# Optimization experiments

Measured on AMD Instinct MI355X. Metric: run time of the kernel, lower is better.

Reference implementation:

```python
import jax, jax.numpy as jnp
import numpy as np

N_NODES = 50000
N_EDGES = 1600000
F_IN = 128
NUM_CLASSES = 40


def _gat_conv(x, src, dst, W, a_src, a_dst, b, concat):
    # x: [N, Fin], W: [Fin, H*C], a_src/a_dst: [H, C], b: [H*C] or [C]
    H, C = a_src.shape
    N = x.shape[0]
    h = (x @ W).reshape(N, H, C)                       # [N,H,C]
    al_s = jnp.einsum('nhc,hc->nh', h, a_src)          # [N,H]
    al_d = jnp.einsum('nhc,hc->nh', h, a_dst)          # [N,H]
    e = jax.nn.leaky_relu(al_s[src] + al_d[dst], 0.2)  # [E,H]
    # segment softmax over destination nodes
    m = jax.ops.segment_max(e, dst, num_segments=N)    # [N,H]
    ex = jnp.exp(e - m[dst])
    s = jax.ops.segment_sum(ex, dst, num_segments=N)   # [N,H]
    alpha = ex / s[dst]                                # [E,H]
    out = jax.ops.segment_sum(h[src] * alpha[:, :, None], dst, num_segments=N)  # [N,H,C]
    if concat:
        return out.reshape(N, H * C) + b
    return out.mean(axis=1) + b


def setup_inputs() -> dict:
    key = jax.random.key(0)
    ks = jax.random.split(key, 12)
    s = 0.1
    inp = {
        'x': jax.random.normal(ks[0], (N_NODES, F_IN), jnp.float32),
        'edge_index': jax.random.randint(ks[1], (2, N_EDGES), 0, N_NODES, jnp.int64),
        # conv1: 128 -> 16, heads=4, concat
        'W1': jax.random.normal(ks[2], (F_IN, 4 * 16), jnp.float32) * s,
        'a1s': jax.random.normal(ks[3], (4, 16), jnp.float32) * s,
        'a1d': jax.random.normal(ks[4], (4, 16), jnp.float32) * s,
        'b1': jnp.zeros((4 * 16,), jnp.float32),
        # conv2: 64 -> 16, heads=4, concat
        'W2': jax.random.normal(ks[5], (64, 4 * 16), jnp.float32) * s,
        'a2s': jax.random.normal(ks[6], (4, 16), jnp.float32) * s,
        'a2d': jax.random.normal(ks[7], (4, 16), jnp.float32) * s,
        'b2': jnp.zeros((4 * 16,), jnp.float32),
        # conv3: 64 -> num_classes, heads=6, mean
        'W3': jax.random.normal(ks[8], (64, 6 * NUM_CLASSES), jnp.float32) * s,
        'a3s': jax.random.normal(ks[9], (6, NUM_CLASSES), jnp.float32) * s,
        'a3d': jax.random.normal(ks[10], (6, NUM_CLASSES), jnp.float32) * s,
        'b3': jnp.zeros((NUM_CLASSES,), jnp.float32),
    }
    return inp


def reference(x, edge_index, W1, a1s, a1d, b1, W2, a2s, a2d, b2, W3, a3s, a3d, b3):
    N = x.shape[0]
    loop = jnp.arange(N, dtype=edge_index.dtype)
    src = jnp.concatenate([edge_index[0], loop])  # add_self_loops=True (PyG default)
    dst = jnp.concatenate([edge_index[1], loop])
    h = jax.nn.elu(_gat_conv(x, src, dst, W1, a1s, a1d, b1, concat=True))
    h = jax.nn.elu(_gat_conv(h, src, dst, W2, a2s, a2d, b2, concat=True))
    h = jax.nn.elu(_gat_conv(h, src, dst, W3, a3s, a3d, b3, concat=False))
    return jax.nn.log_softmax(h, axis=1)
```

## Files before the change

### kernel.cpp

```cpp
#include <hip/hip_runtime.h>
#include <math.h>

#define N_NODES 50000
#define N_EDGES 1600000
#define NB      391
#define CHUNK   8192
#define NCHUNK  196
#define LOG2E   1.44269504088896340736f

typedef __attribute__((ext_vector_type(2))) float v2f;
typedef __attribute__((ext_vector_type(4))) float f32x4;
typedef __attribute__((ext_vector_type(8))) __bf16 bf16x8;

__device__ __forceinline__ float lrelu02(float x) { return fmaxf(x, 0.2f * x); }
__device__ __forceinline__ float elu1(float x)    { return x > 0.f ? x : __expf(x) - 1.f; }
__device__ __forceinline__ float exp2_fast(float x) {
    float r; asm("v_exp_f32 %0, %1" : "=v"(r) : "v"(x)); return r;
}

__device__ __forceinline__ unsigned short f2bf(float f) {
    unsigned int u = __float_as_uint(f);
    return (unsigned short)((u + 0x7fffu + ((u >> 16) & 1u)) >> 16);
}
__device__ __forceinline__ float bf2f(unsigned short s) {
    return __uint_as_float((unsigned int)s << 16);
}
__device__ __forceinline__ float2 bfp2(unsigned int u) {
    float2 r;
    r.x = __uint_as_float(u << 16);
    r.y = __uint_as_float(u & 0xffff0000u);
    return r;
}

union BF8U { unsigned short u[8]; bf16x8 v; };
__device__ __forceinline__ bf16x8 cvt8(float4 a, float4 b) {
    BF8U r;
    r.u[0] = f2bf(a.x); r.u[1] = f2bf(a.y); r.u[2] = f2bf(a.z); r.u[3] = f2bf(a.w);
    r.u[4] = f2bf(b.x); r.u[5] = f2bf(b.y); r.u[6] = f2bf(b.z); r.u[7] = f2bf(b.w);
    return r.v;
}

__global__ __launch_bounds__(256) void bucket2_gemm_kernel(
        const int* __restrict__ ei, int* __restrict__ bcur, unsigned int* __restrict__ stage,
        const float* __restrict__ x, const float* __restrict__ W,
        const float* __restrict__ a_s, const float* __restrict__ a_d,
        unsigned short* __restrict__ h, float* __restrict__ al_s, float* __restrict__ al_d) {
    __shared__ alignas(16) char smem[37472];
    const int tid = threadIdx.x;
    if (blockIdx.x < NCHUNK) {
        unsigned int* vals = (unsigned int*)smem;
        int* hist  = (int*)(smem + 32768);
        int* cnt2  = hist + NB;
        int* gbase = cnt2 + NB;
        for (int i = tid; i < NB; i += 256) { hist[i] = 0; cnt2[i] = 0; }
        __syncthreads();
        const int e0 = blockIdx.x * CHUNK;
        int n = N_EDGES - e0; if (n > CHUNK) n = CHUNK;
        const int4* s4 = (const int4*)ei + (e0 >> 2);
        const int4* d4 = (const int4*)(ei + N_EDGES) + (e0 >> 2);
        for (int i = tid; i < (n >> 2); i += 256) {
            int4 s = s4[i], d = d4[i];
            vals[4 * i + 0] = ((unsigned int)d.x << 16) | (unsigned int)s.x;
            vals[4 * i + 1] = ((unsigned int)d.y << 16) | (unsigned int)s.y;
            vals[4 * i + 2] = ((unsigned int)d.z << 16) | (unsigned int)s.z;
            vals[4 * i + 3] = ((unsigned int)d.w << 16) | (unsigned int)s.w;
            atomicAdd(&hist[d.x >> 7], 1);
            atomicAdd(&hist[d.y >> 7], 1);
            atomicAdd(&hist[d.z >> 7], 1);
            atomicAdd(&hist[d.w >> 7], 1);
        }
        __syncthreads();
        for (int b = tid; b < NB; b += 256)
            if (hist[b]) gbase[b] = atomicAdd(&bcur[b * 16], hist[b]);
        __syncthreads();
        for (int i = tid; i < n; i += 256) {
            unsigned int v = vals[i];
            int b = v >> 23;
            int r = atomicAdd(&cnt2[b], 1);
            stage[gbase[b] + r] = v & 0x7FFFFFu;
        }
    } else {
        constexpr int FIN = 128, KS = FIN / 32;
        unsigned short* Wl = (unsigned short*)smem;
        unsigned short (*ot)[64] = (unsigned short(*)[64])(smem + 16384);
        const int bid = blockIdx.x - NCHUNK;
        for (int i = tid; i < FIN * 64; i += 256) {
            int ks = i >> 11;
            int rem = i & 2047;
            int c = rem >> 5, r = rem & 31;
            Wl[i] = f2bf(W[(ks * 32 + r) * 64 + c]);
        }
        __syncthreads();

        const int wv = tid >> 6, l = tid & 63;
        const int m = l & 15, g = l >> 4;
        const int n0 = bid * 64;
        int row = n0 + wv * 16 + m;
        if (row > N_NODES - 1) row = N_NODES - 1;
        const float* xr = x + (size_t)row * FIN + g * 8;

        f32x4 acc[4] = {};
#pragma unroll
        for (int ks = 0; ks < KS; ++ks) {
            float4 xa = *(const float4*)(xr + ks * 32);
            float4 xb = *(const float4*)(xr + ks * 32 + 4);
            bf16x8 af = cvt8(xa, xb);
            const unsigned short* wp = &Wl[ks * 2048 + g * 8];
#pragma unroll
            for (int t = 0; t < 4; ++t) {
                bf16x8 bf = *(const bf16x8*)(wp + (t * 16 + m) * 32);
                acc[t] = __builtin_amdgcn_mfma_f32_16x16x32_bf16(af, bf, acc[t], 0, 0, 0);
            }
        }
#pragma unroll
        for (int t = 0; t < 4; ++t)
#pragma unroll
            for (int j = 0; j < 4; ++j)
                ot[wv * 16 + g * 4 + j][t * 16 + m] = f2bf(acc[t][j]);
        __syncthreads();

        int vrows = N_NODES - n0; if (vrows > 64) vrows = 64;
        {
            unsigned int* ph = (unsigned int*)(h + (size_t)n0 * 64);
            for (int i = tid; i < vrows * 32; i += 256) {
                int r = i >> 5, c = i & 31;
                ph[i] = *(const unsigned int*)&ot[r][c * 2];
            }
        }
        {
            int node = tid >> 2, hd = tid & 3;
            if (node < vrows) {
                const float* as = a_s + hd * 16;
                const float* ad = a_d + hd * 16;
                float s1 = 0.f, s2 = 0.f;
#pragma unroll
                for (int c = 0; c < 16; c += 2) {
                    unsigned int q = *(const unsigned int*)&ot[node][hd * 16 + c];
                    float2 p = bfp2(q);
                    s1 = fmaf(p.x, as[c], s1);     s2 = fmaf(p.x, ad[c], s2);
                    s1 = fmaf(p.y, as[c + 1], s1); s2 = fmaf(p.y, ad[c + 1], s2);
                }
                al_s[(n0 + node) * 4 + hd] = s1 * LOG2E;
                al_d[(n0 + node) * 4 + hd] = s2 * LOG2E;
            }
        }
    }
}

__global__ __launch_bounds__(256) void gemm_albf64_kernel(const unsigned short* __restrict__ xb,
                               const float* __restrict__ W,
                               const float* __restrict__ a_s, const float* __restrict__ a_d,
                               unsigned short* __restrict__ h,
                               float* __restrict__ al_s, float* __restrict__ al_d) {
    __shared__ alignas(16) unsigned short Wl[2 * 64 * 32];
    __shared__ alignas(16) unsigned short ot[64][64];
    const int tid = threadIdx.x;
    for (int i = tid; i < 64 * 64; i += 256) {
        int ks = i >> 11;
        int rem = i & 2047;
        int c = rem >> 5, r = rem & 31;
        Wl[i] = f2bf(W[(ks * 32 + r) * 64 + c]);
    }
    __syncthreads();

    const int wv = tid >> 6, l = tid & 63;
    const int m = l & 15, g = l >> 4;
    const int n0 = blockIdx.x * 64;
    int row = n0 + wv * 16 + m;
    if (row > N_NODES - 1) row = N_NODES - 1;
    const unsigned short* xr = xb + (size_t)row * 64 + g * 8;

    f32x4 acc[4] = {};
#pragma unroll
    for (int ks = 0; ks < 2; ++ks) {
        bf16x8 af = *(const bf16x8*)(xr + ks * 32);
        const unsigned short* wp = &Wl[ks * 2048 + g * 8];
#pragma unroll
        for (int t = 0; t < 4; ++t) {
            bf16x8 bf = *(const bf16x8*)(wp + (t * 16 + m) * 32);
            acc[t] = __builtin_amdgcn_mfma_f32_16x16x32_bf16(af, bf, acc[t], 0, 0, 0);
        }
    }
#pragma unroll
    for (int t = 0; t < 4; ++t)
#pragma unroll
        for (int j = 0; j < 4; ++j)
            ot[wv * 16 + g * 4 + j][t * 16 + m] = f2bf(acc[t][j]);
    __syncthreads();

    int vrows = N_NODES - n0; if (vrows > 64) vrows = 64;
    {
        unsigned int* ph = (unsigned int*)(h + (size_t)n0 * 64);
        for (int i = tid; i < vrows * 32; i += 256) {
            int r = i >> 5, c = i & 31;
            ph[i] = *(const unsigned int*)&ot[r][c * 2];
        }
    }
    {
        int node = tid >> 2, hd = tid & 3;
        if (node < vrows) {
            const float* as = a_s + hd * 16;
            const float* ad = a_d + hd * 16;
            float s1 = 0.f, s2 = 0.f;
#pragma unroll
            for (int c = 0; c < 16; c += 2) {
                unsigned int q = *(const unsigned int*)&ot[node][hd * 16 + c];
                float2 p = bfp2(q);
                s1 = fmaf(p.x, as[c], s1);     s2 = fmaf(p.x, ad[c], s2);
                s1 = fmaf(p.y, as[c + 1], s1); s2 = fmaf(p.y, ad[c + 1], s2);
            }
            al_s[(n0 + node) * 4 + hd] = s1 * LOG2E;
            al_d[(n0 + node) * 4 + hd] = s2 * LOG2E;
        }
    }
}

__global__ __launch_bounds__(256) void gemm80_kernel(const unsigned short* __restrict__ xb,
                              const float* __restrict__ W,
                              const float* __restrict__ a_s, const float* __restrict__ a_d,
                              unsigned int* __restrict__ h8,
                              float* __restrict__ al_s, float* __restrict__ al_d) {
    __shared__ alignas(16) unsigned short Wl[2 * 80 * 32];
    __shared__ alignas(16) unsigned short ot[64][80];
    const int tid = threadIdx.x;
    const int nb = blockIdx.x / 3, third = blockIdx.x % 3;
    const int cb = third * 80;
    for (int i = tid; i < 2 * 80 * 32; i += 256) {
        int ks = i / 2560;
        int rem = i - ks * 2560;
        int c = rem >> 5, r = rem & 31;
        Wl[i] = f2bf(W[(ks * 32 + r) * 240 + cb + c]);
    }
    __syncthreads();

    const int wv = tid >> 6, l = tid & 63;
    const int m = l & 15, g = l >> 4;
    const int n0 = nb * 64;
    int row = n0 + wv * 16 + m;
    if (row > N_NODES - 1) row = N_NODES - 1;
    const unsigned short* xr = xb + (size_t)row * 64 + g * 8;

    f32x4 acc[5] = {};
#pragma unroll
    for (int ks = 0; ks < 2; ++ks) {
        bf16x8 af = *(const bf16x8*)(xr + ks * 32);
        const unsigned short* wp = &Wl[ks * 2560 + g * 8];
#pragma unroll
        for (int t = 0; t < 5; ++t) {
            bf16x8 bf = *(const bf16x8*)(wp + (t * 16 + m) * 32);
            acc[t] = __builtin_amdgcn_mfma_f32_16x16x32_bf16(af, bf, acc[t], 0, 0, 0);
        }
    }
#pragma unroll
    for (int t = 0; t < 5; ++t)
#pragma unroll
        for (int j = 0; j < 4; ++j)
            ot[wv * 16 + g * 4 + j][t * 16 + m] = f2bf(acc[t][j]);
    __syncthreads();

    int vrows = N_NODES - n0; if (vrows > 64) vrows = 64;
    {
        for (int i = tid; i < vrows * 20; i += 256) {
            int r = i / 20, c = i - r * 20;
            uint2 q = *(const uint2*)&ot[r][c * 4];
            float2 p0 = bfp2(q.x), p1 = bfp2(q.y);
            int lo = __builtin_amdgcn_cvt_pk_fp8_f32(p0.x, p0.y, 0, false);
            unsigned int packed = (unsigned int)__builtin_amdgcn_cvt_pk_fp8_f32(p1.x, p1.y, lo, true);
            h8[(size_t)(n0 + r) * 64 + cb / 4 + c] = packed;
        }
        if (third == 0) {
            for (int i = tid; i < vrows * 4; i += 256)
                h8[(size_t)(n0 + (i >> 2)) * 64 + 60 + (i & 3)] = 0;
        }
    }
    for (int t = tid; t < vrows * 2; t += 256) {
        int node = t >> 1, hh = t & 1;
        int hd = third * 2 + hh;
        const unsigned short* rp = &ot[node][hh * 40];
        const float* as = a_s + hd * 40;
        const float* ad = a_d + hd * 40;
        float s1 = 0.f, s2 = 0.f;
#pragma unroll
        for (int c = 0; c < 40; c += 2) {
            unsigned int q = *(const unsigned int*)(rp + c);
            float2 p = bfp2(q);
            s1 = fmaf(p.x, as[c], s1);     s2 = fmaf(p.x, ad[c], s2);
            s1 = fmaf(p.y, as[c + 1], s1); s2 = fmaf(p.y, ad[c + 1], s2);
        }
        al_s[(n0 + node) * 6 + hd] = s1 * LOG2E;
        al_d[(n0 + node) * 6 + hd] = s2 * LOG2E;
    }
}

__global__ __launch_bounds__(256) void bcnt_kernel(const int* __restrict__ ei, int* __restrict__ bcnt) {
    __shared__ int hist[NB];
    const int t = threadIdx.x;
    for (int i = t; i < NB; i += 256) hist[i] = 0;
    __syncthreads();
    const int e0 = blockIdx.x * CHUNK;
    int n = N_EDGES - e0; if (n > CHUNK) n = CHUNK;
    const int4* d4 = (const int4*)(ei + N_EDGES) + (e0 >> 2);
    for (int i = t; i < (n >> 2); i += 256) {
        int4 d = d4[i];
        atomicAdd(&hist[d.x >> 7], 1);
        atomicAdd(&hist[d.y >> 7], 1);
        atomicAdd(&hist[d.z >> 7], 1);
        atomicAdd(&hist[d.w >> 7], 1);
    }
    __syncthreads();
    for (int b = t; b < NB; b += 256)
        if (hist[b]) atomicAdd(&bcnt[b], hist[b]);
}

__global__ void scan391_kernel(const int* __restrict__ bcnt, int* __restrict__ bbase,
                               int* __restrict__ bcur) {
    __shared__ int wtot[8];
    int b = threadIdx.x;
    int lane = b & 63, w = b >> 6;
    int v = (b < NB) ? bcnt[b] : 0;
    int sc = v;
#pragma unroll
    for (int off = 1; off < 64; off <<= 1) {
        int u = __shfl_up(sc, off);
        if (lane >= off) sc += u;
    }
    if (lane == 63) wtot[w] = sc;
    __syncthreads();
    int add = 0;
    for (int k = 0; k < w; ++k) add += wtot[k];
    int excl = sc - v + add;
    if (b < NB) { bbase[b] = excl; bcur[b * 16] = excl; }
    if (b == 0) bbase[NB] = N_EDGES;
}

__global__ __launch_bounds__(256) void place2_kernel(const unsigned int* __restrict__ stage,
                                                     const int* __restrict__ bbase,
                                                     int* __restrict__ rowptr,
                                                     unsigned short* __restrict__ csr) {
    __shared__ int hist[128];
    __shared__ int cur[128];
    __shared__ int wt[2];
    const int b = blockIdx.x;
    const int n0 = b * 128;
    const int t = threadIdx.x;
    const int base = bbase[b];
    const int endp = bbase[b + 1];
    if (t < 128) hist[t] = 0;
    __syncthreads();
    for (int i = base + t; i < endp; i += 256)
        atomicAdd(&hist[stage[i] >> 16], 1);
    __syncthreads();
    int v = 0, sc = 0;
    if (t < 128) {
        v = hist[t];
        int lane = t & 63, w = t >> 6;
        sc = v;
#pragma unroll
        for (int off = 1; off < 64; off <<= 1) {
            int u = __shfl_up(sc, off);
            if (lane >= off) sc += u;
        }
        if (lane == 63) wt[w] = sc;
    }
    __syncthreads();
    if (t < 128) {
        int add = (t >= 64) ? wt[0] : 0;
        int excl = sc - v + add;
        int n = n0 + t;
        if (n <= N_NODES) rowptr[n] = base + excl;
        cur[t] = base + excl;
    }
    __syncthreads();
    for (int i = base + t; i < endp; i += 256) {
        unsigned int e = stage[i];
        int pos = atomicAdd(&cur[e >> 16], 1);
        csr[pos] = (unsigned short)(e & 0xFFFFu);
    }
}

__global__ void agg64_kernel(const int* __restrict__ rowptr, const unsigned short* __restrict__ csr_src,
                             const float* __restrict__ al_s, const float* __restrict__ al_d,
                             const unsigned short* __restrict__ hb, const float* __restrict__ b,
                             unsigned short* __restrict__ xn) {
    const int node = blockIdx.x * 4 + (threadIdx.x >> 6);
    const int lane = threadIdx.x & 63;
    const int eg = lane >> 3;
    const int cl = lane & 7;
    const int c0 = cl * 8;
    const int hd = cl >> 1;
    const float ald = al_d[(unsigned)(node * 4 + hd)];
    const int beg = rowptr[node], end = rowptr[node + 1];
    float denom = 0.f;
    float a0 = 0.f, a1 = 0.f, a2 = 0.f, a3 = 0.f, a4 = 0.f, a5 = 0.f, a6 = 0.f, a7 = 0.f;
    auto accQ = [&](uint4 q, float w) {
        float2 p;
        p = bfp2(q.x); a0 = fmaf(w, p.x, a0); a1 = fmaf(w, p.y, a1);
        p = bfp2(q.y); a2 = fmaf(w, p.x, a2); a3 = fmaf(w, p.y, a3);
        p = bfp2(q.z); a4 = fmaf(w, p.x, a4); a5 = fmaf(w, p.y, a5);
        p = bfp2(q.w); a6 = fmaf(w, p.x, a6); a7 = fmaf(w, p.y, a7);
    };
    if (eg == 0) {
        float w = exp2_fast(lrelu02(al_s[(unsigned)(node * 4 + hd)] + ald));
        uint4 q = *(const uint4*)(hb + (unsigned)(node * 64 + c0));
        denom = w;
        accQ(q, w);
    }
    int j = beg + eg;
    for (; j + 24 < end; j += 32) {
        int s0 = csr_src[j], s1 = csr_src[j + 8], s2 = csr_src[j + 16], s3 = csr_src[j + 24];
        uint4 q0 = *(const uint4*)(hb + (unsigned)(s0 * 64 + c0));
        uint4 q1 = *(const uint4*)(hb + (unsigned)(s1 * 64 + c0));
        uint4 q2 = *(const uint4*)(hb + (unsigned)(s2 * 64 + c0));
        uint4 q3 = *(const uint4*)(hb + (unsigned)(s3 * 64 + c0));
        float w0 = exp2_fast(lrelu02(al_s[(unsigned)(s0 * 4 + hd)] + ald));
        float w1 = exp2_fast(lrelu02(al_s[(unsigned)(s1 * 4 + hd)] + ald));
        float w2 = exp2_fast(lrelu02(al_s[(unsigned)(s2 * 4 + hd)] + ald));
        float w3 = exp2_fast(lrelu02(al_s[(unsigned)(s3 * 4 + hd)] + ald));
        denom += (w0 + w1) + (w2 + w3);
        accQ(q0, w0); accQ(q1, w1); accQ(q2, w2); accQ(q3, w3);
    }
    for (; j < end; j += 8) {
        int s0 = csr_src[j];
        uint4 q0 = *(const uint4*)(hb + (unsigned)(s0 * 64 + c0));
        float w0 = exp2_fast(lrelu02(al_s[(unsigned)(s0 * 4 + hd)] + ald));
        denom += w0;
        accQ(q0, w0);
    }
    denom += __shfl_xor(denom, 8); denom += __shfl_xor(denom, 16); denom += __shfl_xor(denom, 32);
    a0 += __shfl_xor(a0, 8); a0 += __shfl_xor(a0, 16); a0 += __shfl_xor(a0, 32);
    a1 += __shfl_xor(a1, 8); a1 += __shfl_xor(a1, 16); a1 += __shfl_xor(a1, 32);
    a2 += __shfl_xor(a2, 8); a2 += __shfl_xor(a2, 16); a2 += __shfl_xor(a2, 32);
    a3 += __shfl_xor(a3, 8); a3 += __shfl_xor(a3, 16); a3 += __shfl_xor(a3, 32);
    a4 += __shfl_xor(a4, 8); a4 += __shfl_xor(a4, 16); a4 += __shfl_xor(a4, 32);
    a5 += __shfl_xor(a5, 8); a5 += __shfl_xor(a5, 16); a5 += __shfl_xor(a5, 32);
    a6 += __shfl_xor(a6, 8); a6 += __shfl_xor(a6, 16); a6 += __shfl_xor(a6, 32);
    a7 += __shfl_xor(a7, 8); a7 += __shfl_xor(a7, 16); a7 += __shfl_xor(a7, 32);
    if (lane < 8) {
        float r = 1.f / denom;
        float4 bv0 = *(const float4*)(b + c0);
        float4 bv1 = *(const float4*)(b + c0 + 4);
        uint4 pk;
        pk.x = (unsigned int)f2bf(elu1(fmaf(a0, r, bv0.x)))
             | ((unsigned int)f2bf(elu1(fmaf(a1, r, bv0.y))) << 16);
        pk.y = (unsigned int)f2bf(elu1(fmaf(a2, r, bv0.z)))
             | ((unsigned int)f2bf(elu1(fmaf(a3, r, bv0.w))) << 16);
        pk.z = (unsigned int)f2bf(elu1(fmaf(a4, r, bv1.x)))
             | ((unsigned int)f2bf(elu1(fmaf(a5, r, bv1.y))) << 16);
        pk.w = (unsigned int)f2bf(elu1(fmaf(a6, r, bv1.z)))
             | ((unsigned int)f2bf(elu1(fmaf(a7, r, bv1.w))) << 16);
        *(uint4*)(xn + (unsigned)(node * 64 + c0)) = pk;
    }
}

__global__ void agg240_kernel(const int* __restrict__ rowptr, const unsigned short* __restrict__ csr_src,
                              const float* __restrict__ al_s, const float* __restrict__ al_d,
                              const unsigned int* __restrict__ h8, const float* __restrict__ b3,
                              float* __restrict__ y) {
    __shared__ float sh[4][240];
    const int wv_id = threadIdx.x >> 6;
    const int node = blockIdx.x * 4 + wv_id;
    const int lane = threadIdx.x & 63;
    const int eg = lane >> 5;
    const int cl = lane & 31;
    const int u0 = cl * 2;
    int hd = cl / 5; if (hd > 5) hd = 5;
    const float ald = al_d[(unsigned)(node * 6 + hd)];
    const int beg = rowptr[node], end = rowptr[node + 1];
    float denom = 0.f;
    float acc[8] = {0.f, 0.f, 0.f, 0.f, 0.f, 0.f, 0.f, 0.f};
    auto acc8 = [&](uint2 q, float w) {
        v2f p0 = __builtin_amdgcn_cvt_pk_f32_fp8((int)q.x, false);
        v2f p1 = __builtin_amdgcn_cvt_pk_f32_fp8((int)q.x, true);
        v2f p2 = __builtin_amdgcn_cvt_pk_f32_fp8((int)q.y, false);
        v2f p3 = __builtin_amdgcn_cvt_pk_f32_fp8((int)q.y, true);
        acc[0] = fmaf(w, p0.x, acc[0]); acc[1] = fmaf(w, p0.y, acc[1]);
        acc[2] = fmaf(w, p1.x, acc[2]); acc[3] = fmaf(w, p1.y, acc[3]);
        acc[4] = fmaf(w, p2.x, acc[4]); acc[5] = fmaf(w, p2.y, acc[5]);
        acc[6] = fmaf(w, p3.x, acc[6]); acc[7] = fmaf(w, p3.y, acc[7]);
    };
    if (eg == 0) {
        float w = exp2_fast(lrelu02(al_s[(unsigned)(node * 6 + hd)] + ald));
        uint2 q = *(const uint2*)(h8 + (unsigned)(node * 64) + u0);
        denom = w;
        acc8(q, w);
    }
    int j = beg + eg;
    for (; j + 6 < end; j += 8) {
        int s0 = csr_src[j], s1 = csr_src[j + 2], s2 = csr_src[j + 4], s3 = csr_src[j + 6];
        uint2 q0 = *(const uint2*)(h8 + (unsigned)(s0 * 64) + u0);
        uint2 q1 = *(const uint2*)(h8 + (unsigned)(s1 * 64) + u0);
        uint2 q2 = *(const uint2*)(h8 + (unsigned)(s2 * 64) + u0);
        uint2 q3 = *(const uint2*)(h8 + (unsigned)(s3 * 64) + u0);
        float w0 = exp2_fast(lrelu02(al_s[(unsigned)(s0 * 6 + hd)] + ald));
        float w1 = exp2_fast(lrelu02(al_s[(unsigned)(s1 * 6 + hd)] + ald));
        float w2 = exp2_fast(lrelu02(al_s[(unsigned)(s2 * 6 + hd)] + ald));
        float w3 = exp2_fast(lrelu02(al_s[(unsigned)(s3 * 6 + hd)] + ald));
        denom += (w0 + w1) + (w2 + w3);
        acc8(q0, w0); acc8(q1, w1); acc8(q2, w2); acc8(q3, w3);
    }
    for (; j < end; j += 2) {
        int s0 = csr_src[j];
        uint2 q0 = *(const uint2*)(h8 + (unsigned)(s0 * 64) + u0);
        float w0 = exp2_fast(lrelu02(al_s[(unsigned)(s0 * 6 + hd)] + ald));
        denom += w0;
        acc8(q0, w0);
    }
    denom += __shfl_xor(denom, 32);
#pragma unroll
    for (int i = 0; i < 8; ++i) acc[i] += __shfl_xor(acc[i], 32);
    if (eg == 0 && cl < 30) {
        float r = 1.f / denom;
        float* sp = &sh[wv_id][cl * 8];
#pragma unroll
        for (int i = 0; i < 8; ++i) sp[i] = acc[i] * r;
    }
    __syncthreads();
    float v;
    if (lane < 40) {
        const float* p = sh[wv_id];
        float s = 0.f;
#pragma unroll
        for (int hh = 0; hh < 6; ++hh) s += p[hh * 40 + lane];
        v = elu1(s * (1.f / 6.f) + b3[lane]);
    } else {
        v = -INFINITY;
    }
    float m = v;
#pragma unroll
    for (int o = 32; o > 0; o >>= 1) m = fmaxf(m, __shfl_xor(m, o));
    float ex = (lane < 40) ? __expf(v - m) : 0.f;
    float ssum = ex;
#pragma unroll
    for (int o = 32; o > 0; o >>= 1) ssum += __shfl_xor(ssum, o);
    if (lane < 40) y[(size_t)node * 40 + lane] = v - m - __logf(ssum);
}

extern "C" void kernel_launch(void* const* d_in, const int* in_sizes, int n_in,
                              void* d_out, int out_size, void* d_ws, size_t ws_size,
                              hipStream_t stream) {
    const float* x   = (const float*)d_in[0];
    const int*   ei  = (const int*)d_in[1];
    const float* W1  = (const float*)d_in[2];
    const float* a1s = (const float*)d_in[3];
    const float* a1d = (const float*)d_in[4];
    const float* b1  = (const float*)d_in[5];
    const float* W2  = (const float*)d_in[6];
    const float* a2s = (const float*)d_in[7];
    const float* a2d = (const float*)d_in[8];
    const float* b2  = (const float*)d_in[9];
    const float* W3  = (const float*)d_in[10];
    const float* a3s = (const float*)d_in[11];
    const float* a3d = (const float*)d_in[12];
    const float* b3  = (const float*)d_in[13];
    float* y = (float*)d_out;

    float* ws = (float*)d_ws;
    unsigned short* h_bf = (unsigned short*)ws;
    unsigned short* x_buf = (unsigned short*)(ws + 1600000);
    float* al_s    = ws + 4800000;
    float* al_d    = ws + 5100000;
    unsigned int* h8 = (unsigned int*)(ws + 5400000);
    int*   rowptr  = (int*)(ws + 8600000);
    unsigned short* csr_src = (unsigned short*)(ws + 8650008);
    unsigned int* stage = (unsigned int*)(ws + 9450008);
    int*   bcnt    = (int*)(ws + 11050008);
    int*   bbase   = (int*)(ws + 11050400);
    int*   bcur    = (int*)(ws + 11050792);

    const int agg_grid = N_NODES / 4;
    const int gemm_gx = (N_NODES + 63) / 64;

    hipMemsetAsync(bcnt, 0, NB * sizeof(int), stream);
    bcnt_kernel<<<NCHUNK, 256, 0, stream>>>(ei, bcnt);
    scan391_kernel<<<1, 512, 0, stream>>>(bcnt, bbase, bcur);
    bucket2_gemm_kernel<<<NCHUNK + gemm_gx, 256, 0, stream>>>(ei, bcur, stage,
                                                              x, W1, a1s, a1d, h_bf, al_s, al_d);
    place2_kernel<<<NB, 256, 0, stream>>>(stage, bbase, rowptr, csr_src);

    agg64_kernel<<<agg_grid, 256, 0, stream>>>(rowptr, csr_src, al_s, al_d, h_bf, b1, x_buf);

    gemm_albf64_kernel<<<gemm_gx, 256, 0, stream>>>(x_buf, W2, a2s, a2d, h_bf, al_s, al_d);
    agg64_kernel<<<agg_grid, 256, 0, stream>>>(rowptr, csr_src, al_s, al_d, h_bf, b2, x_buf);

    gemm80_kernel<<<gemm_gx * 3, 256, 0, stream>>>(x_buf, W3, a3s, a3d, h8, al_s, al_d);
    agg240_kernel<<<agg_grid, 256, 0, stream>>>(rowptr, csr_src, al_s, al_d, h8, b3, y);
}
```

Baseline: 335.4 us.

## Spread layer-1 GEMM blocks across bcnt, bucket, and place kernels

```diff
diff --git a/kernel.cpp b/kernel.cpp
--- a/kernel.cpp
+++ b/kernel.cpp
@@ -7,6 +7,9 @@
 #define CHUNK   8192
 #define NCHUNK  196
 #define LOG2E   1.44269504088896340736f
+#define G1A     150
+#define G1B     250
+#define G1C     382
 
 typedef __attribute__((ext_vector_type(2))) float v2f;
 typedef __attribute__((ext_vector_type(4))) float f32x4;
@@ -38,6 +41,126 @@
     r.u[0] = f2bf(a.x); r.u[1] = f2bf(a.y); r.u[2] = f2bf(a.z); r.u[3] = f2bf(a.w);
     r.u[4] = f2bf(b.x); r.u[5] = f2bf(b.y); r.u[6] = f2bf(b.z); r.u[7] = f2bf(b.w);
     return r.v;
+}
+
+__device__ __forceinline__ void gemm1_body(int bid, const float* __restrict__ x,
+        const float* __restrict__ W, const float* __restrict__ a_s, const float* __restrict__ a_d,
+        unsigned short* __restrict__ h, float* __restrict__ al_s, float* __restrict__ al_d,
+        char* smem) {
+    constexpr int FIN = 128, KS = FIN / 32;
+    unsigned short* Wl = (unsigned short*)smem;
+    unsigned short (*ot)[64] = (unsigned short(*)[64])(smem + 16384);
+    const int tid = threadIdx.x;
+    for (int i = tid; i < FIN * 64; i += 256) {
+        int ks = i >> 11;
+        int rem = i & 2047;
+        int c = rem >> 5, r = rem & 31;
+        Wl[i] = f2bf(W[(ks * 32 + r) * 64 + c]);
+    }
+    __syncthreads();
+
+    const int wv = tid >> 6, l = tid & 63;
+    const int m = l & 15, g = l >> 4;
+    const int n0 = bid * 64;
+    int row = n0 + wv * 16 + m;
+    if (row > N_NODES - 1) row = N_NODES - 1;
+    const float* xr = x + (size_t)row * FIN + g * 8;
+
+    f32x4 acc[4] = {};
+#pragma unroll
+    for (int ks = 0; ks < KS; ++ks) {
+        float4 xa = *(const float4*)(xr + ks * 32);
+        float4 xb = *(const float4*)(xr + ks * 32 + 4);
+        bf16x8 af = cvt8(xa, xb);
+        const unsigned short* wp = &Wl[ks * 2048 + g * 8];
+#pragma unroll
+        for (int t = 0; t < 4; ++t) {
+            bf16x8 bf = *(const bf16x8*)(wp + (t * 16 + m) * 32);
+            acc[t] = __builtin_amdgcn_mfma_f32_16x16x32_bf16(af, bf, acc[t], 0, 0, 0);
+        }
+    }
+#pragma unroll
+    for (int t = 0; t < 4; ++t)
+#pragma unroll
+        for (int j = 0; j < 4; ++j)
+            ot[wv * 16 + g * 4 + j][t * 16 + m] = f2bf(acc[t][j]);
+    __syncthreads();
+
+    int vrows = N_NODES - n0; if (vrows > 64) vrows = 64;
+    {
+        unsigned int* ph = (unsigned int*)(h + (size_t)n0 * 64);
+        for (int i = tid; i < vrows * 32; i += 256) {
+            int r = i >> 5, c = i & 31;
+            ph[i] = *(const unsigned int*)&ot[r][c * 2];
+        }
+    }
+    {
+        int node = tid >> 2, hd = tid & 3;
+        if (node < vrows) {
+            const float* as = a_s + hd * 16;
+            const float* ad = a_d + hd * 16;
+            float s1 = 0.f, s2 = 0.f;
+#pragma unroll
+            for (int c = 0; c < 16; c += 2) {
+                unsigned int q = *(const unsigned int*)&ot[node][hd * 16 + c];
+                float2 p = bfp2(q);
+                s1 = fmaf(p.x, as[c], s1);     s2 = fmaf(p.x, ad[c], s2);
+                s1 = fmaf(p.y, as[c + 1], s1); s2 = fmaf(p.y, ad[c + 1], s2);
+            }
+            al_s[(n0 + node) * 4 + hd] = s1 * LOG2E;
+            al_d[(n0 + node) * 4 + hd] = s2 * LOG2E;
+        }
+    }
+}
+
+__global__ __launch_bounds__(256) void bcnt_gemm_kernel(const int* __restrict__ ei,
+        int* __restrict__ bcnt,
+        const float* __restrict__ x, const float* __restrict__ W,
+        const float* __restrict__ a_s, const float* __restrict__ a_d,
+        unsigned short* __restrict__ h, float* __restrict__ al_s, float* __restrict__ al_d) {
+    __shared__ alignas(16) char smem[24576];
+    const int t = threadIdx.x;
+    if (blockIdx.x < NCHUNK) {
+        int* hist = (int*)smem;
+        for (int i = t; i < NB; i += 256) hist[i] = 0;
+        __syncthreads();
+        const int e0 = blockIdx.x * CHUNK;
+        int n = N_EDGES - e0; if (n > CHUNK) n = CHUNK;
+        const int4* d4 = (const int4*)(ei + N_EDGES) + (e0 >> 2);
+        for (int i = t; i < (n >> 2); i += 256) {
+            int4 d = d4[i];
+            atomicAdd(&hist[d.x >> 7], 1);
+            atomicAdd(&hist[d.y >> 7], 1);
+            atomicAdd(&hist[d.z >> 7], 1);
+            atomicAdd(&hist[d.w >> 7], 1);
+        }
+        __syncthreads();
+        for (int b = t; b < NB; b += 256)
+            if (hist[b]) atomicAdd(&bcnt[b], hist[b]);
+    } else {
+        gemm1_body(blockIdx.x - NCHUNK, x, W, a_s, a_d, h, al_s, al_d, smem);
+    }
+}
+
+__global__ void scan391_kernel(const int* __restrict__ bcnt, int* __restrict__ bbase,
+                               int* __restrict__ bcur) {
+    __shared__ int wtot[8];
+    int b = threadIdx.x;
+    int lane = b & 63, w = b >> 6;
+    int v = (b < NB) ? bcnt[b] : 0;
+    int sc = v;
+#pragma unroll
+    for (int off = 1; off < 64; off <<= 1) {
+        int u = __shfl_up(sc, off);
+        if (lane >= off) sc += u;
+    }
+    if (lane == 63) wtot[w] = sc;
+    __syncthreads();
+    int add = 0;
+    for (int k = 0; k < w; ++k) add += wtot[k];
+    int excl = sc - v + add;
+    if (b < NB) { bbase[b] = excl; bcur[b * 16] = excl; }
+    if (b == 0) bbase[NB] = N_EDGES;
 }
 
 __global__ __launch_bounds__(256) void bucket2_gemm_kernel(
@@ -80,70 +203,59 @@
             stage[gbase[b] + r] = v & 0x7FFFFFu;
         }
     } else {
-        constexpr int FIN = 128, KS = FIN / 32;
-        unsigned short* Wl = (unsigned short*)smem;
-        unsigned short (*ot)[64] = (unsigned short(*)[64])(smem + 16384);
-        const int bid = blockIdx.x - NCHUNK;
-        for (int i = tid; i < FIN * 64; i += 256) {
-            int ks = i >> 11;
-            int rem = i & 2047;
-            int c = rem >> 5, r = rem & 31;
-            Wl[i] = f2bf(W[(ks * 32 + r) * 64 + c]);
-        }
-        __syncthreads();
-
-        const int wv = tid >> 6, l = tid & 63;
-        const int m = l & 15, g = l >> 4;
-        const int n0 = bid * 64;
-        int row = n0 + wv * 16 + m;
-        if (row > N_NODES - 1) row = N_NODES - 1;
-        const float* xr = x + (size_t)row * FIN + g * 8;
-
-        f32x4 acc[4] = {};
-#pragma unroll
-        for (int ks = 0; ks < KS; ++ks) {
-            float4 xa = *(const float4*)(xr + ks * 32);
-            float4 xb = *(const float4*)(xr + ks * 32 + 4);
-            bf16x8 af = cvt8(xa, xb);
-            const unsigned short* wp = &Wl[ks * 2048 + g * 8];
-#pragma unroll
-            for (int t = 0; t < 4; ++t) {
-                bf16x8 bf = *(const bf16x8*)(wp + (t * 16 + m) * 32);
-                acc[t] = __builtin_amdgcn_mfma_f32_16x16x32_bf16(af, bf, acc[t], 0, 0, 0);
+        gemm1_body(blockIdx.x - NCHUNK + G1A, x, W, a_s, a_d, h, al_s, al_d, smem);
+    }
+}
+
+__global__ __launch_bounds__(256) void place2_gemm_kernel(
+        const unsigned int* __restrict__ stage, const int* __restrict__ bbase,
+        int* __restrict__ rowptr, unsigned short* __restrict__ csr,
+        const float* __restrict__ x, const float* __restrict__ W,
+        const float* __restrict__ a_s, const float* __restrict__ a_d,
+        unsigned short* __restrict__ h, float* __restrict__ al_s, float* __restrict__ al_d) {
+    __shared__ alignas(16) char smem[24576];
+    const int t = threadIdx.x;
+    if (blockIdx.x < NB) {
+        int* hist = (int*)smem;
+        int* cur  = hist + 128;
+        int* wt   = cur + 128;
+        const int b = blockIdx.x;
+        const int n0 = b * 128;
+        const int base = bbase[b];
+        const int endp = bbase[b + 1];
+        if (t < 128) hist[t] = 0;
+        __syncthreads();
+        for (int i = base + t; i < endp; i += 256)
+            atomicAdd(&hist[stage[i] >> 16], 1);
+        __syncthreads();
+        int v = 0, sc = 0;
+        if (t < 128) {
+            v = hist[t];
+            int lane = t & 63, w = t >> 6;
+            sc = v;
+#pragma unroll
+            for (int off = 1; off < 64; off <<= 1) {
+                int u = __shfl_up(sc, off);
+                if (lane >= off) sc += u;
             }
-        }
-#pragma unroll
-        for (int t = 0; t < 4; ++t)
-#pragma unroll
-            for (int j = 0; j < 4; ++j)
-                ot[wv * 16 + g * 4 + j][t * 16 + m] = f2bf(acc[t][j]);
-        __syncthreads();
-
-        int vrows = N_NODES - n0; if (vrows > 64) vrows = 64;
-        {
-            unsigned int* ph = (unsigned int*)(h + (size_t)n0 * 64);
-            for (int i = tid; i < vrows * 32; i += 256) {
-                int r = i >> 5, c = i & 31;
-                ph[i] = *(const unsigned int*)&ot[r][c * 2];
-            }
-        }
-        {
-            int node = tid >> 2, hd = tid & 3;
-            if (node < vrows) {
-                const float* as = a_s + hd * 16;
-                const float* ad = a_d + hd * 16;
-                float s1 = 0.f, s2 = 0.f;
-#pragma unroll
-                for (int c = 0; c < 16; c += 2) {
-                    unsigned int q = *(const unsigned int*)&ot[node][hd * 16 + c];
-                    float2 p = bfp2(q);
-                    s1 = fmaf(p.x, as[c], s1);     s2 = fmaf(p.x, ad[c], s2);
-                    s1 = fmaf(p.y, as[c + 1], s1); s2 = fmaf(p.y, ad[c + 1], s2);
-                }
-                al_s[(n0 + node) * 4 + hd] = s1 * LOG2E;
-                al_d[(n0 + node) * 4 + hd] = s2 * LOG2E;
-            }
-        }
+            if (lane == 63) wt[w] = sc;
+        }
+        __syncthreads();
+        if (t < 128) {
+            int add = (t >= 64) ? wt[0] : 0;
+            int excl = sc - v + add;
+            int n = n0 + t;
+            if (n <= N_NODES) rowptr[n] = base + excl;
+            cur[t] = base + excl;
+        }
+        __syncthreads();
+        for (int i = base + t; i < endp; i += 256) {
+            unsigned int e = stage[i];
+            int pos = atomicAdd(&cur[e >> 16], 1);
+            csr[pos] = (unsigned short)(e & 0xFFFFu);
+        }
+    } else {
+        gemm1_body(blockIdx.x - NB + G1A + G1B, x, W, a_s, a_d, h, al_s, al_d, smem);
     }
 }
 
@@ -289,92 +401,6 @@
         }
         al_s[(n0 + node) * 6 + hd] = s1 * LOG2E;
         al_d[(n0 + node) * 6 + hd] = s2 * LOG2E;
-    }
-}
-
-__global__ __launch_bounds__(256) void bcnt_kernel(const int* __restrict__ ei, int* __restrict__ bcnt) {
-    __shared__ int hist[NB];
-    const int t = threadIdx.x;
-    for (int i = t; i < NB; i += 256) hist[i] = 0;
-    __syncthreads();
-    const int e0 = blockIdx.x * CHUNK;
-    int n = N_EDGES - e0; if (n > CHUNK) n = CHUNK;
-    const int4* d4 = (const int4*)(ei + N_EDGES) + (e0 >> 2);
-    for (int i = t; i < (n >> 2); i += 256) {
-        int4 d = d4[i];
-        atomicAdd(&hist[d.x >> 7], 1);
-        atomicAdd(&hist[d.y >> 7], 1);
-        atomicAdd(&hist[d.z >> 7], 1);
-        atomicAdd(&hist[d.w >> 7], 1);
-    }
-    __syncthreads();
-    for (int b = t; b < NB; b += 256)
-        if (hist[b]) atomicAdd(&bcnt[b], hist[b]);
-}
-
-__global__ void scan391_kernel(const int* __restrict__ bcnt, int* __restrict__ bbase,
-                               int* __restrict__ bcur) {
-    __shared__ int wtot[8];
-    int b = threadIdx.x;
-    int lane = b & 63, w = b >> 6;
-    int v = (b < NB) ? bcnt[b] : 0;
-    int sc = v;
-#pragma unroll
-    for (int off = 1; off < 64; off <<= 1) {
-        int u = __shfl_up(sc, off);
-        if (lane >= off) sc += u;
-    }
-    if (lane == 63) wtot[w] = sc;
-    __syncthreads();
-    int add = 0;
-    for (int k = 0; k < w; ++k) add += wtot[k];
-    int excl = sc - v + add;
-    if (b < NB) { bbase[b] = excl; bcur[b * 16] = excl; }
-    if (b == 0) bbase[NB] = N_EDGES;
-}
-
-__global__ __launch_bounds__(256) void place2_kernel(const unsigned int* __restrict__ stage,
-                                                     const int* __restrict__ bbase,
-                                                     int* __restrict__ rowptr,
-                                                     unsigned short* __restrict__ csr) {
-    __shared__ int hist[128];
-    __shared__ int cur[128];
-    __shared__ int wt[2];
-    const int b = blockIdx.x;
-    const int n0 = b * 128;
-    const int t = threadIdx.x;
-    const int base = bbase[b];
-    const int endp = bbase[b + 1];
-    if (t < 128) hist[t] = 0;
-    __syncthreads();
-    for (int i = base + t; i < endp; i += 256)
-        atomicAdd(&hist[stage[i] >> 16], 1);
-    __syncthreads();
-    int v = 0, sc = 0;
-    if (t < 128) {
-        v = hist[t];
-        int lane = t & 63, w = t >> 6;
-        sc = v;
-#pragma unroll
-        for (int off = 1; off < 64; off <<= 1) {
-            int u = __shfl_up(sc, off);
-            if (lane >= off) sc += u;
-        }
-        if (lane == 63) wt[w] = sc;
-    }
-    __syncthreads();
-    if (t < 128) {
-        int add = (t >= 64) ? wt[0] : 0;
-        int excl = sc - v + add;
-        int n = n0 + t;
-        if (n <= N_NODES) rowptr[n] = base + excl;
-        cur[t] = base + excl;
-    }
-    __syncthreads();
-    for (int i = base + t; i < endp; i += 256) {
-        unsigned int e = stage[i];
-        int pos = atomicAdd(&cur[e >> 16], 1);
-        csr[pos] = (unsigned short)(e & 0xFFFFu);
     }
 }
 
@@ -571,11 +597,13 @@
     const int gemm_gx = (N_NODES + 63) / 64;
 
     hipMemsetAsync(bcnt, 0, NB * sizeof(int), stream);
-    bcnt_kernel<<<NCHUNK, 256, 0, stream>>>(ei, bcnt);
+    bcnt_gemm_kernel<<<NCHUNK + G1A, 256, 0, stream>>>(ei, bcnt,
+                                                       x, W1, a1s, a1d, h_bf, al_s, al_d);
     scan391_kernel<<<1, 512, 0, stream>>>(bcnt, bbase, bcur);
-    bucket2_gemm_kernel<<<NCHUNK + gemm_gx, 256, 0, stream>>>(ei, bcur, stage,
-                                                              x, W1, a1s, a1d, h_bf, al_s, al_d);
-    place2_kernel<<<NB, 256, 0, stream>>>(stage, bbase, rowptr, csr_src);
+    bucket2_gemm_kernel<<<NCHUNK + G1B, 256, 0, stream>>>(ei, bcur, stage,
+                                                          x, W1, a1s, a1d, h_bf, al_s, al_d);
+    place2_gemm_kernel<<<NB + G1C, 256, 0, stream>>>(stage, bbase, rowptr, csr_src,
+                                                     x, W1, a1s, a1d, h_bf, al_s, al_d);
 
     agg64_kernel<<<agg_grid, 256, 0, stream>>>(rowptr, csr_src, al_s, al_d, h_bf, b1, x_buf);
 
```

Measured after the change: 332.8 us. Within noise of the previous version (-0.8%).
